# Kernel optimization log

Hardware: AMD Instinct MI355X
Metric: run time of the kernel (lower is better)

Reference implementation:

```python
import jax, jax.numpy as jnp
import numpy as np

N = 50000   # nodes
E = 800000  # edges (avg degree 16)
D = 128     # in_channels == num_hidden_channels


def setup_inputs() -> dict:
    key = jax.random.key(0)
    ks = jax.random.split(key, 8)
    embs = jax.random.normal(ks[0], (N, D), dtype=jnp.float32)
    edge_index0 = jax.random.randint(ks[1], (2, E), 0, N)
    edge_index1 = jax.random.randint(ks[2], (2, E), 0, N)
    s = 1.0 / np.sqrt(D)  # torch Linear default init bound
    Wl0 = jax.random.uniform(ks[3], (D, D), jnp.float32, -s, s)
    Wr0 = jax.random.uniform(ks[4], (D, D), jnp.float32, -s, s)
    bl0 = jax.random.uniform(ks[5], (D,), jnp.float32, -s, s)
    Wl1 = jax.random.uniform(ks[6], (D, D), jnp.float32, -s, s)
    Wr1 = jax.random.uniform(ks[7], (D, D), jnp.float32, -s, s)
    bl1 = jnp.zeros((D,), jnp.float32)
    return {"embs": embs, "edge_index0": edge_index0, "edge_index1": edge_index1,
            "Wl0": Wl0, "bl0": bl0, "Wr0": Wr0, "Wl1": Wl1, "bl1": bl1, "Wr1": Wr1}


def sage_conv(x, edge_index, Wl, bl, Wr):
    # PyG SAGEConv, aggr='mean': out = lin_l(mean_{j->i} x_j) + lin_r(x_i)
    src, dst = edge_index[0], edge_index[1]
    msg = x[src]  # [E, D] gather of source-node features
    agg = jax.ops.segment_sum(msg, dst, num_segments=x.shape[0])            # [N, D]
    cnt = jax.ops.segment_sum(jnp.ones((src.shape[0],), x.dtype), dst,
                              num_segments=x.shape[0])                      # [N]
    mean = agg / jnp.maximum(cnt, 1.0)[:, None]  # isolated nodes -> 0 (scatter_mean)
    return mean @ Wl + bl + x @ Wr


def reference(embs, edge_index0, edge_index1, Wl0, bl0, Wr0, Wl1, bl1, Wr1):
    # outer layer 0 (not last) -> conv, dropout (eval: identity), exact GELU
    x = sage_conv(embs, edge_index0, Wl0, bl0, Wr0)
    x = jax.nn.gelu(x, approximate=False)
    # outer layer 1 (last) -> conv only
    x = sage_conv(x, edge_index1, Wl1, bl1, Wr1)
    return x
```

## Files before the change

### kernel.cpp

```cpp
#include <hip/hip_runtime.h>
#include <math.h>

#define D 128
#define BKT_SHIFT 8
#define CHUNK 4096
#define CAP 5120

typedef __attribute__((ext_vector_type(8))) short bf8;
typedef __attribute__((ext_vector_type(4))) float f4;

__device__ __forceinline__ float b2f(ushort u) {
    union { uint i; float f; } x; x.i = ((uint)u) << 16; return x.f;
}
__device__ __forceinline__ ushort f2b(float f) {
    union { float f; uint i; } x; x.f = f;
    uint i = x.i;
    i += 0x7fffu + ((i >> 16) & 1u);
    return (ushort)(i >> 16);
}

__global__ void cvt_bf16(const float* __restrict__ in, ushort* __restrict__ outb, long n4) {
    long i = (long)blockIdx.x * blockDim.x + threadIdx.x;
    long stride = (long)gridDim.x * blockDim.x;
    for (; i < n4; i += stride) {
        float4 v = ((const float4*)in)[i];
        ushort4 o = { f2b(v.x), f2b(v.y), f2b(v.z), f2b(v.w) };
        ((ushort4*)outb)[i] = o;
    }
}

__global__ void wt_bf16(const float* __restrict__ W0, const float* __restrict__ W1,
                        const float* __restrict__ W2, const float* __restrict__ W3,
                        ushort* __restrict__ WT, int* __restrict__ gbc) {
    __shared__ ushort s[128][132];
    const float* W = blockIdx.x == 0 ? W0 : blockIdx.x == 1 ? W1 : blockIdx.x == 2 ? W2 : W3;
    ushort* o = WT + (long)blockIdx.x * D * D;
    int t = threadIdx.x;
    if (blockIdx.x == 0) { gbc[t] = 0; gbc[256 + t] = 0; }
    for (int i = t; i < D * D; i += 256) { int k = i >> 7, c = i & 127; s[k][c] = f2b(W[i]); }
    __syncthreads();
    for (int i = t; i < D * D; i += 256) { int c = i >> 7, k = i & 127; o[i] = s[k][c]; }
}

__global__ __launch_bounds__(256)
void bucket_scatter(const int* __restrict__ ei0, const int* __restrict__ ei1, int E,
                    int* __restrict__ gbc, uint* __restrict__ tmpf) {
    const int* ei = blockIdx.y ? ei1 : ei0;
    int* cnts = gbc + blockIdx.y * 256;
    uint* tp = tmpf + (size_t)blockIdx.y * 256 * CAP;
    __shared__ int lhist[256], lstart[256], lcur[256], gbase[256];
    __shared__ int ws[4];
    __shared__ uint sw[CHUNK];
    const int t = threadIdx.x;
    const int e0 = blockIdx.x * CHUNK;
    const int cnt = min(CHUNK, E - e0);
    lhist[t] = 0;
    __syncthreads();
    for (int i = t; i < cnt; i += 256)
        atomicAdd(&lhist[ei[E + e0 + i] >> BKT_SHIFT], 1);
    __syncthreads();
    {
        int lane = t & 63, wid = t >> 6;
        int v = lhist[t];
        int incl = v;
        #pragma unroll
        for (int o = 1; o < 64; o <<= 1) { int u = __shfl_up(incl, o); if (lane >= o) incl += u; }
        if (lane == 63) ws[wid] = incl;
        __syncthreads();
        int wb = 0;
        #pragma unroll
        for (int w = 0; w < 3; ++w) if (w < wid) wb += ws[w];
        int excl = incl - v + wb;
        lstart[t] = excl;
        lcur[t] = excl;
    }
    __syncthreads();
    for (int i = t; i < cnt; i += 256) {
        int s = ei[e0 + i];
        int d = ei[E + e0 + i];
        int r = atomicAdd(&lcur[d >> BKT_SHIFT], 1);
        sw[r] = ((uint)d << 16) | (uint)s;
    }
    __syncthreads();
    gbase[t] = lhist[t] > 0 ? atomicAdd(&cnts[t], lhist[t]) : 0;
    __syncthreads();
    for (int i = t; i < cnt; i += 256) {
        uint w = sw[i];
        int b = w >> 24;
        tp[(size_t)b * CAP + gbase[b] + (i - lstart[b])] = w;
    }
}

__global__ __launch_bounds__(256)
void exact_place(const uint* __restrict__ tmpf, const int* __restrict__ gbc,
                 int* __restrict__ o0, int* __restrict__ o1,
                 int* __restrict__ d0, int* __restrict__ d1,
                 ushort* __restrict__ s0, ushort* __restrict__ s1, int N) {
    const int layer = blockIdx.y;
    const uint* tp = tmpf + ((size_t)layer * 256 + blockIdx.x) * CAP;
    int* offs = layer ? o1 : o0;
    int* deg  = layer ? d1 : d0;
    ushort* srcs = layer ? s1 : s0;
    __shared__ int lh[256], lc[256], sbase[256];
    __shared__ int ws[4];
    const int t = threadIdx.x;
    const int lane = t & 63, wid = t >> 6;
    const int node0 = blockIdx.x << BKT_SHIFT;

    {
        int v = gbc[layer * 256 + t];
        int incl = v;
        #pragma unroll
        for (int o = 1; o < 64; o <<= 1) { int u = __shfl_up(incl, o); if (lane >= o) incl += u; }
        if (lane == 63) ws[wid] = incl;
        __syncthreads();
        int wb = 0;
        #pragma unroll
        for (int w = 0; w < 3; ++w) if (w < wid) wb += ws[w];
        sbase[t] = incl - v + wb;
        lh[t] = 0;
    }
    __syncthreads();
    const int bstart = sbase[blockIdx.x];
    const int cnt = gbc[layer * 256 + blockIdx.x];

    for (int i = t; i < cnt; i += 256)
        atomicAdd(&lh[(tp[i] >> 16) & 255], 1);
    __syncthreads();
    {
        int v = lh[t];
        int incl = v;
        #pragma unroll
        for (int o = 1; o < 64; o <<= 1) { int u = __shfl_up(incl, o); if (lane >= o) incl += u; }
        if (lane == 63) ws[wid] = incl;
        __syncthreads();
        int wb = 0;
        #pragma unroll
        for (int w = 0; w < 3; ++w) if (w < wid) wb += ws[w];
        int excl = incl - v + wb;
        int node = node0 + t;
        if (node < N) { offs[node] = bstart + excl; deg[node] = v; }
        lc[t] = bstart + excl;
    }
    __syncthreads();
    for (int i = t; i < cnt; i += 256) {
        uint w = tp[i];
        int p = atomicAdd(&lc[(w >> 16) & 255], 1);
        srcs[p] = (ushort)(w & 0xffff);
    }
}

__global__ void gather_mean_b(const ushort* __restrict__ xb, const ushort* __restrict__ srcs,
                              const int* __restrict__ offs, const int* __restrict__ deg,
                              ushort* __restrict__ meanb, int N) {
    int node = blockIdx.x * (blockDim.x >> 6) + (threadIdx.x >> 6);
    if (node >= N) return;
    int lane = threadIdx.x & 63;
    int g = lane >> 4;
    int c = (lane & 15) * 8;
    int beg = offs[node], dc = deg[node];
    int end = beg + dc;
    float a[8] = {0.f, 0.f, 0.f, 0.f, 0.f, 0.f, 0.f, 0.f};
    int e = beg + g;
    for (; e + 4 < end; e += 8) {
        int s0 = srcs[e];
        int s1 = srcs[e + 4];
        bf8 v0 = *(const bf8*)(xb + (long)s0 * D + c);
        bf8 v1 = *(const bf8*)(xb + (long)s1 * D + c);
        #pragma unroll
        for (int q = 0; q < 8; ++q) a[q] += b2f((ushort)v0[q]) + b2f((ushort)v1[q]);
    }
    if (e < end) {
        int s0 = srcs[e];
        bf8 v0 = *(const bf8*)(xb + (long)s0 * D + c);
        #pragma unroll
        for (int q = 0; q < 8; ++q) a[q] += b2f((ushort)v0[q]);
    }
    #pragma unroll
    for (int q = 0; q < 8; ++q) {
        a[q] += __shfl_xor(a[q], 16);
        a[q] += __shfl_xor(a[q], 32);
    }
    if (g == 0) {
        float inv = dc > 0 ? 1.0f / (float)dc : 0.0f;
        bf8 o;
        #pragma unroll
        for (int q = 0; q < 8; ++q) o[q] = (short)f2b(a[q] * inv);
        *(bf8*)(meanb + (long)node * D + c) = o;
    }
}

template <int ACT>
__global__ __launch_bounds__(256, 2)
void gemm_mfma(const ushort* __restrict__ meanb, const ushort* __restrict__ xb,
               const ushort* __restrict__ WTl, const ushort* __restrict__ WTr,
               const float* __restrict__ bias, float* __restrict__ outf,
               ushort* __restrict__ outb, int N) {
    __shared__ ushort sW[2 * D * D];
    const int t = threadIdx.x;
    const int lane = t & 63;
    const int wid  = t >> 6;

    #pragma unroll
    for (int i = 0; i < 16; ++i) {
        const ushort* Wsrc = (i < 8) ? WTl : WTr;
        int off = (t << 4) + (i & 7) * 4096;
        int row = off >> 8;
        int dst = ((i < 8) ? 0 : 32768) + (off ^ ((row & 7) << 4));
        *(bf8*)((char*)sW + dst) = *(const bf8*)((const char*)Wsrc + off);
    }

    const int r0   = blockIdx.x * 128 + wid * 32;
    const int arow = r0 + (lane & 15);
    const int kg   = lane >> 4;
    bf8 z = {};
    bf8 am[8], ax[8];
    #pragma unroll
    for (int m = 0; m < 4; ++m) {
        const long a0 = (long)arow * D + kg * 8 + m * 32;
        if (arow < N)      { am[m]   = *(const bf8*)(meanb + a0);
                             ax[m]   = *(const bf8*)(xb + a0); }
        else               { am[m]   = z; ax[m]   = z; }
        if (arow + 16 < N) { am[m+4] = *(const bf8*)(meanb + a0 + 16 * D);
                             ax[m+4] = *(const bf8*)(xb + a0 + 16 * D); }
        else               { am[m+4] = z; ax[m+4] = z; }
    }

    const int sxor = (lane & 7) << 4;
    int p[4];
    #pragma unroll
    for (int m = 0; m < 4; ++m)
        p[m] = (lane & 15) * 256 + ((kg * 16 + m * 64) ^ sxor);

    __syncthreads();

    f4 acc0[8], acc1[8];
    #pragma unroll
    for (int n = 0; n < 8; ++n) { acc0[n] = (f4){0.f,0.f,0.f,0.f}; acc1[n] = (f4){0.f,0.f,0.f,0.f}; }

    #pragma unroll
    for (int m = 0; m < 4; ++m) {
        #pragma unroll
        for (int n = 0; n < 8; ++n) {
            bf8 bl = *(const bf8*)((const char*)sW + n * 4096 + p[m]);
            acc0[n] = __builtin_amdgcn_mfma_f32_16x16x32_bf16(am[m],     bl, acc0[n], 0, 0, 0);
            acc1[n] = __builtin_amdgcn_mfma_f32_16x16x32_bf16(am[m + 4], bl, acc1[n], 0, 0, 0);
        }
    }
    #pragma unroll
    for (int m = 0; m < 4; ++m) {
        #pragma unroll
        for (int n = 0; n < 8; ++n) {
            bf8 br = *(const bf8*)((const char*)sW + 32768 + n * 4096 + p[m]);
            acc0[n] = __builtin_amdgcn_mfma_f32_16x16x32_bf16(ax[m],     br, acc0[n], 0, 0, 0);
            acc1[n] = __builtin_amdgcn_mfma_f32_16x16x32_bf16(ax[m + 4], br, acc1[n], 0, 0, 0);
        }
    }

    const int col0  = lane & 15;
    const int orow0 = r0 + kg * 4;
    #pragma unroll
    for (int n = 0; n < 8; ++n) {
        const int col = n * 16 + col0;
        const float b = bias[col];
        #pragma unroll
        for (int r = 0; r < 4; ++r) {
            #pragma unroll
            for (int h = 0; h < 2; ++h) {
                const int row = orow0 + r + h * 16;
                if (row >= N) continue;
                float v = (h ? acc1[n][r] : acc0[n][r]) + b;
                if (ACT) {
                    v = 0.5f * v * (1.0f + erff(v * 0.70710678118654752f));
                    outb[(long)row * D + col] = f2b(v);
                } else {
                    outf[(long)row * D + col] = v;
                }
            }
        }
    }
}

extern "C" void kernel_launch(void* const* d_in, const int* in_sizes, int n_in,
                              void* d_out, int out_size, void* d_ws, size_t ws_size,
                              hipStream_t stream) {
    const float* embs = (const float*)d_in[0];
    const int*   ei0  = (const int*)d_in[1];
    const int*   ei1  = (const int*)d_in[2];
    const float* Wl0  = (const float*)d_in[3];
    const float* bl0  = (const float*)d_in[4];
    const float* Wr0  = (const float*)d_in[5];
    const float* Wl1  = (const float*)d_in[6];
    const float* bl1  = (const float*)d_in[7];
    const float* Wr1  = (const float*)d_in[8];

    const int N = in_sizes[0] / D;
    const int E = in_sizes[1] / 2;
    float* out = (float*)d_out;

    char* w = (char*)d_ws;
    ushort* xb    = (ushort*)w;  w += (size_t)N * D * 2;
    ushort* meanb = (ushort*)w;  w += (size_t)N * D * 2;
    ushort* WT    = (ushort*)w;  w += (size_t)4 * D * D * 2;
    int* gbc      = (int*)w;     w += 512 * 4;
    int* offs0    = (int*)w;     w += (size_t)N * 4;
    int* offs1    = (int*)w;     w += (size_t)N * 4;
    int* deg0     = (int*)w;     w += (size_t)N * 4;
    int* deg1     = (int*)w;     w += (size_t)N * 4;
    uint* tmpf    = (uint*)w;    w += (size_t)2 * 256 * CAP * 4;
    ushort* srcs0 = (ushort*)w;  w += (size_t)E * 2;
    ushort* srcs1 = (ushort*)w;

    ushort* WTl0 = WT;
    ushort* WTr0 = WT + D * D;
    ushort* WTl1 = WT + 2 * D * D;
    ushort* WTr1 = WT + 3 * D * D;

    const int nbkt = (N + 255) >> BKT_SHIFT;
    const int ncnk = (E + CHUNK - 1) / CHUNK;
    const int ab   = (N + 3) / 4;
    const int gb   = (N + 127) / 128;

    cvt_bf16<<<2048, 256, 0, stream>>>(embs, xb, (long)N * D / 4);
    wt_bf16<<<4, 256, 0, stream>>>(Wl0, Wr0, Wl1, Wr1, WT, gbc);

    bucket_scatter<<<dim3(ncnk, 2), 256, 0, stream>>>(ei0, ei1, E, gbc, tmpf);
    exact_place<<<dim3(nbkt, 2), 256, 0, stream>>>(tmpf, gbc, offs0, offs1,
                                                   deg0, deg1, srcs0, srcs1, N);

    gather_mean_b<<<ab, 256, 0, stream>>>(xb, srcs0, offs0, deg0, meanb, N);
    gemm_mfma<1><<<gb, 256, 0, stream>>>(meanb, xb, WTl0, WTr0, bl0, nullptr, xb, N);

    gather_mean_b<<<ab, 256, 0, stream>>>(xb, srcs1, offs1, deg1, meanb, N);
    gemm_mfma<0><<<gb, 256, 0, stream>>>(meanb, xb, WTl1, WTr1, bl1, out, nullptr, N);
}
```

Before: 148.8 us.

## Fuse prep kernels, unroll gather by four, use 512-thread GEMM blocks

Merges the weight transpose/convert kernel and the embedding bf16 conversion into one launch, so one kernel launch is saved. Adds a 4-way unrolled edge loop in the mean-gather to keep more independent row loads in flight per lane. Doubles the GEMM block to 512 threads covering 256 rows, so each block's shared-memory weight load is shared across more rows. The larger GEMM blocks may reduce occupancy and change register limits, since the launch-bounds min-blocks hint is dropped.

```diff
diff --git a/kernel.cpp b/kernel.cpp
--- a/kernel.cpp
+++ b/kernel.cpp
@@ -19,27 +19,29 @@
     return (ushort)(i >> 16);
 }
 
-__global__ void cvt_bf16(const float* __restrict__ in, ushort* __restrict__ outb, long n4) {
-    long i = (long)blockIdx.x * blockDim.x + threadIdx.x;
-    long stride = (long)gridDim.x * blockDim.x;
+__global__ __launch_bounds__(256)
+void prep_fused(const float* __restrict__ embs, ushort* __restrict__ xb, long n4,
+                const float* __restrict__ W0, const float* __restrict__ W1,
+                const float* __restrict__ W2, const float* __restrict__ W3,
+                ushort* __restrict__ WT, int* __restrict__ gbc) {
+    const int t = threadIdx.x;
+    if (blockIdx.x < 4) {
+        __shared__ ushort s[128][132];
+        const float* W = blockIdx.x == 0 ? W0 : blockIdx.x == 1 ? W1 : blockIdx.x == 2 ? W2 : W3;
+        ushort* o = WT + (long)blockIdx.x * D * D;
+        if (blockIdx.x == 0) { gbc[t] = 0; gbc[256 + t] = 0; }
+        for (int i = t; i < D * D; i += 256) { int k = i >> 7, c = i & 127; s[k][c] = f2b(W[i]); }
+        __syncthreads();
+        for (int i = t; i < D * D; i += 256) { int c = i >> 7, k = i & 127; o[i] = s[k][c]; }
+        return;
+    }
+    long i = (long)(blockIdx.x - 4) * blockDim.x + t;
+    long stride = (long)(gridDim.x - 4) * blockDim.x;
     for (; i < n4; i += stride) {
-        float4 v = ((const float4*)in)[i];
+        float4 v = ((const float4*)embs)[i];
         ushort4 o = { f2b(v.x), f2b(v.y), f2b(v.z), f2b(v.w) };
-        ((ushort4*)outb)[i] = o;
-    }
-}
-
-__global__ void wt_bf16(const float* __restrict__ W0, const float* __restrict__ W1,
-                        const float* __restrict__ W2, const float* __restrict__ W3,
-                        ushort* __restrict__ WT, int* __restrict__ gbc) {
-    __shared__ ushort s[128][132];
-    const float* W = blockIdx.x == 0 ? W0 : blockIdx.x == 1 ? W1 : blockIdx.x == 2 ? W2 : W3;
-    ushort* o = WT + (long)blockIdx.x * D * D;
-    int t = threadIdx.x;
-    if (blockIdx.x == 0) { gbc[t] = 0; gbc[256 + t] = 0; }
-    for (int i = t; i < D * D; i += 256) { int k = i >> 7, c = i & 127; s[k][c] = f2b(W[i]); }
-    __syncthreads();
-    for (int i = t; i < D * D; i += 256) { int c = i >> 7, k = i & 127; o[i] = s[k][c]; }
+        ((ushort4*)xb)[i] = o;
+    }
 }
 
 __global__ __launch_bounds__(256)
@@ -162,6 +164,20 @@
     int end = beg + dc;
     float a[8] = {0.f, 0.f, 0.f, 0.f, 0.f, 0.f, 0.f, 0.f};
     int e = beg + g;
+    for (; e + 12 < end; e += 16) {
+        int s0 = srcs[e];
+        int s1 = srcs[e + 4];
+        int s2 = srcs[e + 8];
+        int s3 = srcs[e + 12];
+        bf8 v0 = *(const bf8*)(xb + (long)s0 * D + c);
+        bf8 v1 = *(const bf8*)(xb + (long)s1 * D + c);
+        bf8 v2 = *(const bf8*)(xb + (long)s2 * D + c);
+        bf8 v3 = *(const bf8*)(xb + (long)s3 * D + c);
+        #pragma unroll
+        for (int q = 0; q < 8; ++q)
+            a[q] += (b2f((ushort)v0[q]) + b2f((ushort)v1[q]))
+                  + (b2f((ushort)v2[q]) + b2f((ushort)v3[q]));
+    }
     for (; e + 4 < end; e += 8) {
         int s0 = srcs[e];
         int s1 = srcs[e + 4];
@@ -191,7 +207,7 @@
 }
 
 template <int ACT>
-__global__ __launch_bounds__(256, 2)
+__global__ __launch_bounds__(512)
 void gemm_mfma(const ushort* __restrict__ meanb, const ushort* __restrict__ xb,
                const ushort* __restrict__ WTl, const ushort* __restrict__ WTr,
                const float* __restrict__ bias, float* __restrict__ outf,
@@ -202,15 +218,15 @@
     const int wid  = t >> 6;
 
     #pragma unroll
-    for (int i = 0; i < 16; ++i) {
-        const ushort* Wsrc = (i < 8) ? WTl : WTr;
-        int off = (t << 4) + (i & 7) * 4096;
+    for (int i = 0; i < 8; ++i) {
+        const ushort* Wsrc = (i < 4) ? WTl : WTr;
+        int off = (t << 4) + (i & 3) * 8192;
         int row = off >> 8;
-        int dst = ((i < 8) ? 0 : 32768) + (off ^ ((row & 7) << 4));
+        int dst = ((i < 4) ? 0 : 32768) + (off ^ ((row & 7) << 4));
         *(bf8*)((char*)sW + dst) = *(const bf8*)((const char*)Wsrc + off);
     }
 
-    const int r0   = blockIdx.x * 128 + wid * 32;
+    const int r0   = blockIdx.x * 256 + wid * 32;
     const int arow = r0 + (lane & 15);
     const int kg   = lane >> 4;
     bf8 z = {};
@@ -319,18 +335,18 @@
     const int nbkt = (N + 255) >> BKT_SHIFT;
     const int ncnk = (E + CHUNK - 1) / CHUNK;
     const int ab   = (N + 3) / 4;
-    const int gb   = (N + 127) / 128;
-
-    cvt_bf16<<<2048, 256, 0, stream>>>(embs, xb, (long)N * D / 4);
-    wt_bf16<<<4, 256, 0, stream>>>(Wl0, Wr0, Wl1, Wr1, WT, gbc);
+    const int gb   = (N + 255) / 256;
+
+    prep_fused<<<2052, 256, 0, stream>>>(embs, xb, (long)N * D / 4,
+                                         Wl0, Wr0, Wl1, Wr1, WT, gbc);
 
     bucket_scatter<<<dim3(ncnk, 2), 256, 0, stream>>>(ei0, ei1, E, gbc, tmpf);
     exact_place<<<dim3(nbkt, 2), 256, 0, stream>>>(tmpf, gbc, offs0, offs1,
                                                    deg0, deg1, srcs0, srcs1, N);
 
     gather_mean_b<<<ab, 256, 0, stream>>>(xb, srcs0, offs0, deg0, meanb, N);
-    gemm_mfma<1><<<gb, 256, 0, stream>>>(meanb, xb, WTl0, WTr0, bl0, nullptr, xb, N);
+    gemm_mfma<1><<<gb, 512, 0, stream>>>(meanb, xb, WTl0, WTr0, bl0, nullptr, xb, N);
 
     gather_mean_b<<<ab, 256, 0, stream>>>(xb, srcs1, offs1, deg1, meanb, N);
-    gemm_mfma<0><<<gb, 256, 0, stream>>>(meanb, xb, WTl1, WTr1, bl1, out, nullptr, N);
-}
+    gemm_mfma<0><<<gb, 512, 0, stream>>>(meanb, xb, WTl1, WTr1, bl1, out, nullptr, N);
+}
```

Measured after the change: 141.3 us. -5.0%, faster.
